# Kernel tuning notes

Measured on AMD Instinct MI355X. Metric: run time of the kernel, lower is better.

Reference implementation:

```python
import jax, jax.numpy as jnp
import numpy as np

N_USERS = 4096
N_ITEMS = 4096
D = 64  # embedding_dim / out_features
N = N_USERS + N_ITEMS
ALPHA = 0.2  # LeakyReLU slope
NEG_INF = jnp.float32(-9e15)


def setup_inputs() -> dict:
    key = jax.random.key(0)
    ks = jax.random.split(key, 11)
    s = 0.05  # xavier-ish scale
    rn = lambda k, shape: jax.random.normal(k, shape, jnp.float32) * s
    adj = jax.random.randint(ks[0], (N, N), 0, 2, jnp.int32)
    return {
        "adj": adj,
        "user_emb": rn(ks[1], (N_USERS, D)),
        "item_emb": rn(ks[2], (N_ITEMS, D)),
        "W0_w": rn(ks[3], (D, D)), "W0_b": rn(ks[4], (D,)), "a0": rn(ks[5], (2 * D, 1)),
        "W1_w": rn(ks[6], (D, D)), "W1_b": rn(ks[7], (D,)), "a1": rn(ks[8], (2 * D, 1)),
        "out_w": rn(ks[9], (D, D)), "out_b": rn(ks[10], (D,)),
    }


def gat_layer(x, adj, W_w, W_b, a):
    # Wh: [N, D]
    Wh = x @ W_w.T + W_b
    # Original materializes [N,N,2D] concat then matmul with a.
    # Algebraically identical: e_ij = leakyrelu(a1 . Wh_i + a2 . Wh_j)
    src = Wh @ a[:D]          # [N, 1] -> row contribution
    dst = (Wh @ a[D:]).T      # [1, N] -> column contribution
    e = jax.nn.leaky_relu(src + dst, ALPHA)        # [N, N]
    e = jnp.where(adj > 0, e, NEG_INF)
    att = jax.nn.softmax(e, axis=1)                # dropout=0.0 (eval)
    return att @ Wh                                 # [N, D]


def reference(adj, user_emb, item_emb, W0_w, W0_b, a0, W1_w, W1_b, a1, out_w, out_b):
    x = jnp.concatenate([user_emb, item_emb], axis=0)  # [N, D]
    x = jax.nn.relu(gat_layer(x, adj, W0_w, W0_b, a0))
    x = jax.nn.relu(gat_layer(x, adj, W1_w, W1_b, a1))
    u, it = x[:N_USERS], x[N_USERS:]
    return (u @ out_w.T + out_b, it @ out_w.T + out_b)
```

## Files before the change

### kernel.cpp

```cpp
#include <hip/hip_runtime.h>


typedef _Float16 f16x8 __attribute__((ext_vector_type(8)));
typedef _Float16 f16x2 __attribute__((ext_vector_type(2)));
typedef __attribute__((ext_vector_type(4))) float f32x4;

union Frag16 {
    f16x8        v;
    unsigned int u[4];
};
union HV2 {
    f16x2        v;
    _Float16     h[2];
    unsigned int u;
};

__device__ __forceinline__ void prep_tail(
    float (*xs)[65], float (*Wt)[65], float (*sred)[64], float (*dred)[64],
    const float* __restrict__ W, const float* __restrict__ bias,
    const float* __restrict__ avec,
    _Float16* __restrict__ WhT,
    unsigned int* __restrict__ E12,
    _Float16* __restrict__ F1h, _Float16* __restrict__ F2h,
    int tid, int r0)
{
    for (int e = tid; e < 4096; e += 256) {
        int o = e >> 6, c = e & 63;
        Wt[c][o] = W[e];
    }
    __syncthreads();

    int r = tid & 63, chunk = tid >> 6, c0 = chunk * 16;
    float acc[16];
#pragma unroll
    for (int o = 0; o < 16; o++) acc[o] = bias[c0 + o];
    for (int c = 0; c < 64; c++) {
        float xv = xs[r][c];
#pragma unroll
        for (int o = 0; o < 16; o++) acc[o] += xv * Wt[c][c0 + o];
    }

    float sp = 0.f, dp = 0.f;
#pragma unroll
    for (int o = 0; o < 16; o++) {
        sp += acc[o] * avec[c0 + o];
        dp += acc[o] * avec[64 + c0 + o];
    }
    sred[chunk][r] = sp;
    dred[chunk][r] = dp;

#pragma unroll
    for (int o = 0; o < 16; o++)
        WhT[(size_t)(c0 + o) * 8192 + r0 + r] = (_Float16)acc[o];

    __syncthreads();
    if (tid < 64) {
        int g = r0 + tid;
        float s = sred[0][tid] + sred[1][tid] + sred[2][tid] + sred[3][tid];
        float d = dred[0][tid] + dred[1][tid] + dred[2][tid] + dred[3][tid];
        HV2 e;
        e.h[0] = (_Float16)__expf(s);
        e.h[1] = (_Float16)__expf(0.2f * s);
        E12[g] = e.u;
        F1h[g] = (_Float16)__expf(d);
        F2h[g] = (_Float16)__expf(0.2f * d);
    }
}

__global__ __launch_bounds__(256) void k_prep0(
    const float* __restrict__ ue, const float* __restrict__ ie,
    const float* __restrict__ W, const float* __restrict__ bias,
    const float* __restrict__ avec,
    _Float16* __restrict__ WhT, unsigned int* __restrict__ E12,
    _Float16* __restrict__ F1h, _Float16* __restrict__ F2h)
{
    __shared__ float xs[64][65];
    __shared__ float Wt[64][65];
    __shared__ float sred[4][64];
    __shared__ float dred[4][64];
    int tid = threadIdx.x, r0 = blockIdx.x * 64;

    for (int e = tid; e < 4096; e += 256) {
        int r = e >> 6, c = e & 63;
        int row = r0 + r;
        xs[r][c] = (row < 4096) ? ue[row * 64 + c] : ie[(row - 4096) * 64 + c];
    }
    prep_tail(xs, Wt, sred, dred, W, bias, avec, WhT, E12, F1h, F2h, tid, r0);
}

template <int NS>
__global__ __launch_bounds__(256) void k_prep1(
    const float* __restrict__ numP, const float* __restrict__ denP,
    const float* __restrict__ W, const float* __restrict__ bias,
    const float* __restrict__ avec,
    _Float16* __restrict__ WhT, unsigned int* __restrict__ E12,
    _Float16* __restrict__ F1h, _Float16* __restrict__ F2h)
{
    __shared__ float xs[64][65];
    __shared__ float Wt[64][65];
    __shared__ float sred[4][64];
    __shared__ float dred[4][64];
    __shared__ float dtot[64];
    int tid = threadIdx.x, r0 = blockIdx.x * 64;
    int rowblk = blockIdx.x;

    if (tid < 64) {
        float s = 0.f;
#pragma unroll
        for (int p = 0; p < NS; p++) s += denP[p * 8192 + r0 + tid];
        dtot[tid] = fmaxf(s, 1e-20f);
    }
    __syncthreads();
    for (int e = tid; e < 4096; e += 256) {
        int r = e >> 6;
        float s = 0.f;
#pragma unroll
        for (int p = 0; p < NS; p++)
            s += numP[(size_t)(p * 128 + rowblk) * 4096 + e];
        float v = s / dtot[r];
        xs[r][e & 63] = v > 0.f ? v : 0.f;
    }
    prep_tail(xs, Wt, sred, dred, W, bias, avec, WhT, E12, F1h, F2h, tid, r0);
}

struct AggSmem {
    union {
        _Float16 WhB[64][136];
        struct {
            float T[64][68];
            float denT[64];
        } ep;
    } u;
    unsigned int mkAll[64][36];
    unsigned int f1All[512];
    unsigned int f2All[512];
};

template <int RAW>
__global__ __launch_bounds__(256) void k_agg(
    const int* __restrict__ adj, unsigned int* __restrict__ bits,
    const _Float16* __restrict__ WhT, const unsigned int* __restrict__ E12,
    const _Float16* __restrict__ F1h, const _Float16* __restrict__ F2h,
    float* __restrict__ numP, float* __restrict__ denP)
{
    constexpr int CK = 128, NCH = 8;
    __shared__ AggSmem sm;

    int tid  = threadIdx.x;
    int wave = tid >> 6, lane = tid & 63;
    int quad = lane >> 4, l16 = lane & 15;
    int rowblk = blockIdx.x, ks = blockIdx.y;
    int k0 = ks * (CK * NCH);

    if constexpr (RAW) {
        for (int r = 0; r < 16; r++) {
            int row_l = wave * 16 + r;
            const int* ap = adj + (size_t)(rowblk * 64 + row_l) * 8192 + k0 + lane;
            int a[16];
#pragma unroll
            for (int g = 0; g < 16; g++) a[g] = ap[g * 64];
            unsigned long long mb[16];
#pragma unroll
            for (int g = 0; g < 16; g++) mb[g] = __ballot(a[g] != 0);
            if (lane == 0) {
#pragma unroll
                for (int g = 0; g < 16; g++) {
                    sm.mkAll[row_l][2 * g]     = (unsigned int)mb[g];
                    sm.mkAll[row_l][2 * g + 1] = (unsigned int)(mb[g] >> 32);
                }
            }
        }
        __syncthreads();
        for (int t = tid; t < 512; t += 256) {
            int row_l = t >> 3, w4 = (t & 7) * 4;
            uint4 v = *reinterpret_cast<const uint4*>(&sm.mkAll[row_l][w4]);
            *reinterpret_cast<uint4*>(
                bits + (size_t)(rowblk * 64 + row_l) * 256 + ks * 32 + w4) = v;
        }
    } else {
        for (int t = tid; t < 512; t += 256) {
            int row_l = t >> 3, w4 = (t & 7) * 4;
            uint4 v = *reinterpret_cast<const uint4*>(
                bits + (size_t)(rowblk * 64 + row_l) * 256 + ks * 32 + w4);
            *reinterpret_cast<uint4*>(&sm.mkAll[row_l][w4]) = v;
        }
    }
    if (tid < 128) {
        uint4 v = *reinterpret_cast<const uint4*>(F1h + k0 + tid * 8);
        *reinterpret_cast<uint4*>(&sm.f1All[tid * 4]) = v;
    } else {
        int t2 = tid - 128;
        uint4 v = *reinterpret_cast<const uint4*>(F2h + k0 + t2 * 8);
        *reinterpret_cast<uint4*>(&sm.f2All[t2 * 4]) = v;
    }

    uint4 P[4];
#pragma unroll
    for (int i = 0; i < 4; i++) {
        int p = tid + 256 * i, f = p >> 4, c8 = (p & 15) * 8;
        P[i] = *reinterpret_cast<const uint4*>(WhT + (size_t)f * 8192 + k0 + c8);
    }
#pragma unroll
    for (int i = 0; i < 4; i++) {
        int p = tid + 256 * i, f = p >> 4, c8 = (p & 15) * 8;
        *reinterpret_cast<uint4*>(&sm.u.WhB[f][c8]) = P[i];
    }
    __syncthreads();

    int row = rowblk * 64 + wave * 16 + l16;
    int lrow = wave * 16 + l16;
    unsigned int e12 = E12[row];
    HV2 e1p, e2p;
    e1p.u = (e12 & 0xFFFFu);  e1p.u |= e1p.u << 16;
    e2p.u = (e12 >> 16);      e2p.u |= e2p.u << 16;

    f32x4 accs[4];
    f32x4 accd = {0.f, 0.f, 0.f, 0.f};
#pragma unroll
    for (int nt = 0; nt < 4; nt++) accs[nt] = accd;

    Frag16 ones;
    ones.u[0] = ones.u[1] = ones.u[2] = ones.u[3] = 0x3C003C00u;

    for (int c = 0; c < NCH; c++) {
        if (c + 1 < NCH) {
            int kc = k0 + (c + 1) * CK;
#pragma unroll
            for (int i = 0; i < 4; i++) {
                int p = tid + 256 * i, f = p >> 4, c8 = (p & 15) * 8;
                P[i] = *reinterpret_cast<const uint4*>(
                    WhT + (size_t)f * 8192 + kc + c8);
            }
        }

#pragma unroll
        for (int kb = 0; kb < CK; kb += 32) {
            int kq = kb + quad * 8;
            unsigned int word = sm.mkAll[lrow][c * 4 + (kb >> 5)];
            unsigned int w8 = word >> (quad * 8);

            int fidx = (c * CK + kq) >> 1;
            uint4 f1v = *reinterpret_cast<const uint4*>(&sm.f1All[fidx]);
            uint4 f2v = *reinterpret_cast<const uint4*>(&sm.f2All[fidx]);
            unsigned int f1a[4] = {f1v.x, f1v.y, f1v.z, f1v.w};
            unsigned int f2a[4] = {f2v.x, f2v.y, f2v.z, f2v.w};

            Frag16 A;
#pragma unroll
            for (int p = 0; p < 4; p++) {
                HV2 fa, fb, wa;
                fa.u = f1a[p];
                fb.u = f2a[p];
                wa.v = __builtin_elementwise_max(e1p.v * fa.v, e2p.v * fb.v);
                int s0 = ((int)(w8 << (31 - 2 * p))) >> 31;
                int s1 = ((int)(w8 << (30 - 2 * p))) >> 31;
                unsigned int pm = ((unsigned)s0 & 0xFFFFu) | ((unsigned)s1 << 16);
                A.u[p] = wa.u & pm;
            }

#pragma unroll
            for (int nt = 0; nt < 4; nt++) {
                Frag16 B;
                B.v = *reinterpret_cast<const f16x8*>(&sm.u.WhB[nt * 16 + l16][kq]);
                accs[nt] = __builtin_amdgcn_mfma_f32_16x16x32_f16(A.v, B.v,
                                                                  accs[nt], 0, 0, 0);
            }
            accd = __builtin_amdgcn_mfma_f32_16x16x32_f16(A.v, ones.v, accd, 0, 0, 0);
        }

        if (c + 1 < NCH) {
            __syncthreads();
#pragma unroll
            for (int i = 0; i < 4; i++) {
                int p = tid + 256 * i, f = p >> 4, c8 = (p & 15) * 8;
                *reinterpret_cast<uint4*>(&sm.u.WhB[f][c8]) = P[i];
            }
            __syncthreads();
        }
    }

    __syncthreads();
#pragma unroll
    for (int rr = 0; rr < 4; rr++) {
        int r = wave * 16 + quad * 4 + rr;
#pragma unroll
        for (int nt = 0; nt < 4; nt++)
            sm.u.ep.T[r][nt * 16 + l16] = accs[nt][rr];
        if (l16 == 0) sm.u.ep.denT[r] = accd[rr];
    }
    __syncthreads();

    float* dst = numP + (size_t)(ks * 128 + rowblk) * 4096;
#pragma unroll
    for (int i = 0; i < 4; i++) {
        int idx = i * 1024 + tid * 4;
        int r = idx >> 6, c2 = idx & 63;
        float4 v = *reinterpret_cast<const float4*>(&sm.u.ep.T[r][c2]);
        *reinterpret_cast<float4*>(dst + idx) = v;
    }
    if (tid < 64)
        denP[ks * 8192 + rowblk * 64 + tid] = sm.u.ep.denT[tid];
}

template <int NS>
__global__ __launch_bounds__(256) void k_out(
    const float* __restrict__ numP, const float* __restrict__ denP,
    const float* __restrict__ W, const float* __restrict__ bias,
    float* __restrict__ out)
{
    __shared__ float xs[64][65];
    __shared__ float Wt[64][65];
    __shared__ float dtot[64];
    int tid = threadIdx.x, r0 = blockIdx.x * 64;
    int rowblk = blockIdx.x;

    if (tid < 64) {
        float s = 0.f;
#pragma unroll
        for (int p = 0; p < NS; p++) s += denP[p * 8192 + r0 + tid];
        dtot[tid] = fmaxf(s, 1e-20f);
    }
    __syncthreads();
    for (int e = tid; e < 4096; e += 256) {
        int r = e >> 6;
        float s = 0.f;
#pragma unroll
        for (int p = 0; p < NS; p++)
            s += numP[(size_t)(p * 128 + rowblk) * 4096 + e];
        float v = s / dtot[r];
        xs[r][e & 63] = v > 0.f ? v : 0.f;
    }
    for (int e = tid; e < 4096; e += 256) {
        int o = e >> 6, c = e & 63;
        Wt[c][o] = W[e];
    }
    __syncthreads();

    int r = tid & 63, chunk = tid >> 6, c0 = chunk * 16;
    float acc[16];
#pragma unroll
    for (int o = 0; o < 16; o++) acc[o] = bias[c0 + o];
    for (int c = 0; c < 64; c++) {
        float xv = xs[r][c];
#pragma unroll
        for (int o = 0; o < 16; o++) acc[o] += xv * Wt[c][c0 + o];
    }
#pragma unroll
    for (int o = 0; o < 16; o++)
        out[(r0 + r) * 64 + c0 + o] = acc[o];
}

extern "C" void kernel_launch(void* const* d_in, const int* in_sizes, int n_in,
                              void* d_out, int out_size, void* d_ws, size_t ws_size,
                              hipStream_t stream)
{
    const int*   adj = (const int*)d_in[0];
    const float* ue  = (const float*)d_in[1];
    const float* ie  = (const float*)d_in[2];
    const float* W0w = (const float*)d_in[3];
    const float* W0b = (const float*)d_in[4];
    const float* a0  = (const float*)d_in[5];
    const float* W1w = (const float*)d_in[6];
    const float* W1b = (const float*)d_in[7];
    const float* a1  = (const float*)d_in[8];
    const float* Ow  = (const float*)d_in[9];
    const float* Ob  = (const float*)d_in[10];

    constexpr int NS = 8;

    char* ws = (char*)d_ws;
    size_t off = 0;
    auto alloc = [&](size_t bytes) -> char* {
        char* p = ws + off;
        off += (bytes + 255) & ~(size_t)255;
        return p;
    };
    float*        numP    = (float*)alloc((size_t)NS * 524288 * 4);
    float*        denP    = (float*)alloc((size_t)NS * 8192 * 4);
    unsigned int* adjbits = (unsigned int*)alloc(8192 * 1024);
    _Float16*     WhT0    = (_Float16*)alloc(64 * 8192 * 2);
    _Float16*     WhT1    = (_Float16*)alloc(64 * 8192 * 2);
    unsigned int* E12_0   = (unsigned int*)alloc(8192 * 4);
    unsigned int* E12_1   = (unsigned int*)alloc(8192 * 4);
    _Float16* F1h0 = (_Float16*)alloc(8192 * 2);
    _Float16* F2h0 = (_Float16*)alloc(8192 * 2);
    _Float16* F1h1 = (_Float16*)alloc(8192 * 2);
    _Float16* F2h1 = (_Float16*)alloc(8192 * 2);

    k_prep0<<<128, 256, 0, stream>>>(ue, ie, W0w, W0b, a0,
                                     WhT0, E12_0, F1h0, F2h0);
    k_agg<1><<<dim3(128, NS), 256, 0, stream>>>(adj, adjbits, WhT0, E12_0,
                                                F1h0, F2h0, numP, denP);
    k_prep1<NS><<<128, 256, 0, stream>>>(numP, denP, W1w, W1b, a1,
                                         WhT1, E12_1, F1h1, F2h1);
    k_agg<0><<<dim3(128, NS), 256, 0, stream>>>(adj, adjbits, WhT1, E12_1,
                                                F1h1, F2h1, numP, denP);
    k_out<NS><<<128, 256, 0, stream>>>(numP, denP, Ow, Ob, (float*)d_out);
}
```

Measured before the change: 514.4 us.

## Split adjacency bit-packing into a standalone kernel and double K-split count

Moves the int32-to-bitmask packing of the adjacency matrix out of the first aggregation kernel into a dedicated grid-stride kernel that uses all CUs with coalesced reads. Halves the per-block K chunk (NCH 8→4) and doubles the split count NS to 16, so each aggregation launch has 2048 blocks instead of 1024 and better occupancy. The shared-memory tile padding is also adjusted. In exchange there is an extra launch, and the partial-sum traffic and reduction work in prep1/out double with the larger NS.

Measured after the change: 511.0 us. About the same (-0.7%).

```diff
diff --git a/kernel.cpp b/kernel.cpp
--- a/kernel.cpp
+++ b/kernel.cpp
@@ -14,6 +14,27 @@
     _Float16     h[2];
     unsigned int u;
 };
+
+__global__ __launch_bounds__(256) void k_pack(
+    const int* __restrict__ adj, unsigned long long* __restrict__ bits)
+{
+    int wgid = blockIdx.x * 4 + (threadIdx.x >> 6);
+    int lane = threadIdx.x & 63;
+    const long long NW  = 2048LL * 4;
+    const long long TOT = 8192LL * 8192;
+    for (long long base = (long long)wgid * 512; base < TOT; base += NW * 512) {
+        int a[8];
+#pragma unroll
+        for (int i = 0; i < 8; i++) a[i] = adj[base + i * 64 + lane];
+        unsigned long long m[8];
+#pragma unroll
+        for (int i = 0; i < 8; i++) m[i] = __ballot(a[i] != 0);
+        if (lane < 4) {
+            reinterpret_cast<ulonglong2*>(bits + (base >> 6))[lane] =
+                ulonglong2{m[2 * lane], m[2 * lane + 1]};
+        }
+    }
+}
 
 __device__ __forceinline__ void prep_tail(
     float (*xs)[65], float (*Wt)[65], float (*sred)[64], float (*dred)[64],
@@ -125,25 +146,24 @@
 
 struct AggSmem {
     union {
-        _Float16 WhB[64][136];
+        _Float16 WhB[64][138];
         struct {
             float T[64][68];
             float denT[64];
         } ep;
     } u;
-    unsigned int mkAll[64][36];
-    unsigned int f1All[512];
-    unsigned int f2All[512];
+    unsigned int mkAll[64][20];
+    unsigned int f1All[256];
+    unsigned int f2All[256];
 };
 
-template <int RAW>
-__global__ __launch_bounds__(256) void k_agg(
-    const int* __restrict__ adj, unsigned int* __restrict__ bits,
+__device__ __forceinline__ void agg_body(
+    const unsigned int* __restrict__ bits,
     const _Float16* __restrict__ WhT, const unsigned int* __restrict__ E12,
     const _Float16* __restrict__ F1h, const _Float16* __restrict__ F2h,
     float* __restrict__ numP, float* __restrict__ denP)
 {
-    constexpr int CK = 128, NCH = 8;
+    constexpr int CK = 128, NCH = 4;
     __shared__ AggSmem sm;
 
     int tid  = threadIdx.x;
@@ -152,44 +172,17 @@
     int rowblk = blockIdx.x, ks = blockIdx.y;
     int k0 = ks * (CK * NCH);
 
-    if constexpr (RAW) {
-        for (int r = 0; r < 16; r++) {
-            int row_l = wave * 16 + r;
-            const int* ap = adj + (size_t)(rowblk * 64 + row_l) * 8192 + k0 + lane;
-            int a[16];
-#pragma unroll
-            for (int g = 0; g < 16; g++) a[g] = ap[g * 64];
-            unsigned long long mb[16];
-#pragma unroll
-            for (int g = 0; g < 16; g++) mb[g] = __ballot(a[g] != 0);
-            if (lane == 0) {
-#pragma unroll
-                for (int g = 0; g < 16; g++) {
-                    sm.mkAll[row_l][2 * g]     = (unsigned int)mb[g];
-                    sm.mkAll[row_l][2 * g + 1] = (unsigned int)(mb[g] >> 32);
-                }
-            }
-        }
-        __syncthreads();
-        for (int t = tid; t < 512; t += 256) {
-            int row_l = t >> 3, w4 = (t & 7) * 4;
-            uint4 v = *reinterpret_cast<const uint4*>(&sm.mkAll[row_l][w4]);
-            *reinterpret_cast<uint4*>(
-                bits + (size_t)(rowblk * 64 + row_l) * 256 + ks * 32 + w4) = v;
-        }
-    } else {
-        for (int t = tid; t < 512; t += 256) {
-            int row_l = t >> 3, w4 = (t & 7) * 4;
-            uint4 v = *reinterpret_cast<const uint4*>(
-                bits + (size_t)(rowblk * 64 + row_l) * 256 + ks * 32 + w4);
-            *reinterpret_cast<uint4*>(&sm.mkAll[row_l][w4]) = v;
-        }
-    }
-    if (tid < 128) {
+    {
+        int row_l = tid >> 2, w4 = (tid & 3) * 4;
+        uint4 v = *reinterpret_cast<const uint4*>(
+            bits + (size_t)(rowblk * 64 + row_l) * 256 + ks * 16 + w4);
+        *reinterpret_cast<uint4*>(&sm.mkAll[row_l][w4]) = v;
+    }
+    if (tid < 64) {
         uint4 v = *reinterpret_cast<const uint4*>(F1h + k0 + tid * 8);
         *reinterpret_cast<uint4*>(&sm.f1All[tid * 4]) = v;
-    } else {
-        int t2 = tid - 128;
+    } else if (tid < 128) {
+        int t2 = tid - 64;
         uint4 v = *reinterpret_cast<const uint4*>(F2h + k0 + t2 * 8);
         *reinterpret_cast<uint4*>(&sm.f2All[t2 * 4]) = v;
     }
@@ -300,6 +293,24 @@
     }
     if (tid < 64)
         denP[ks * 8192 + rowblk * 64 + tid] = sm.u.ep.denT[tid];
+}
+
+__global__ __launch_bounds__(256) void k_agg_l0(
+    const unsigned int* __restrict__ bits,
+    const _Float16* __restrict__ WhT, const unsigned int* __restrict__ E12,
+    const _Float16* __restrict__ F1h, const _Float16* __restrict__ F2h,
+    float* __restrict__ numP, float* __restrict__ denP)
+{
+    agg_body(bits, WhT, E12, F1h, F2h, numP, denP);
+}
+
+__global__ __launch_bounds__(256) void k_agg_l1(
+    const unsigned int* __restrict__ bits,
+    const _Float16* __restrict__ WhT, const unsigned int* __restrict__ E12,
+    const _Float16* __restrict__ F1h, const _Float16* __restrict__ F2h,
+    float* __restrict__ numP, float* __restrict__ denP)
+{
+    agg_body(bits, WhT, E12, F1h, F2h, numP, denP);
 }
 
 template <int NS>
@@ -366,7 +377,7 @@
     const float* Ow  = (const float*)d_in[9];
     const float* Ob  = (const float*)d_in[10];
 
-    constexpr int NS = 8;
+    constexpr int NS = 16;
 
     char* ws = (char*)d_ws;
     size_t off = 0;
@@ -377,7 +388,7 @@
     };
     float*        numP    = (float*)alloc((size_t)NS * 524288 * 4);
     float*        denP    = (float*)alloc((size_t)NS * 8192 * 4);
-    unsigned int* adjbits = (unsigned int*)alloc(8192 * 1024);
+    unsigned long long* adjbits = (unsigned long long*)alloc(8192 * 1024);
     _Float16*     WhT0    = (_Float16*)alloc(64 * 8192 * 2);
     _Float16*     WhT1    = (_Float16*)alloc(64 * 8192 * 2);
     unsigned int* E12_0   = (unsigned int*)alloc(8192 * 4);
@@ -387,13 +398,17 @@
     _Float16* F1h1 = (_Float16*)alloc(8192 * 2);
     _Float16* F2h1 = (_Float16*)alloc(8192 * 2);
 
+    const unsigned int* bits32 = (const unsigned int*)adjbits;
+
+    k_pack<<<2048, 256, 0, stream>>>(adj, adjbits);
+
     k_prep0<<<128, 256, 0, stream>>>(ue, ie, W0w, W0b, a0,
                                      WhT0, E12_0, F1h0, F2h0);
-    k_agg<1><<<dim3(128, NS), 256, 0, stream>>>(adj, adjbits, WhT0, E12_0,
+    k_agg_l0<<<dim3(128, NS), 256, 0, stream>>>(bits32, WhT0, E12_0,
                                                 F1h0, F2h0, numP, denP);
     k_prep1<NS><<<128, 256, 0, stream>>>(numP, denP, W1w, W1b, a1,
                                          WhT1, E12_1, F1h1, F2h1);
-    k_agg<0><<<dim3(128, NS), 256, 0, stream>>>(adj, adjbits, WhT1, E12_1,
+    k_agg_l1<<<dim3(128, NS), 256, 0, stream>>>(bits32, WhT1, E12_1,
                                                 F1h1, F2h1, numP, denP);
     k_out<NS><<<128, 256, 0, stream>>>(numP, denP, Ow, Ob, (float*)d_out);
 }
```
